# Performance work log

Measured on AMD Instinct MI355X. Metric: run time of the kernel, lower is better.

Reference implementation:

```python
import jax, jax.numpy as jnp
import numpy as np

B, U, D, H = 8, 256, 512, 32

def _layernorm(x, g, b, eps=1e-5):
    m = jnp.mean(x, axis=-1, keepdims=True)
    v = jnp.var(x, axis=-1, keepdims=True)
    return (x - m) * jax.lax.rsqrt(v + eps) * g + b

def setup_inputs() -> dict:
    key = jax.random.key(0)
    ks = jax.random.split(key, 12)
    s = 0.02
    return {
        "z_dyn": jax.random.normal(ks[0], (B, U, D), jnp.float32),
        "z_sem": jax.random.normal(ks[1], (B, U, D), jnp.float32),
        "te_w": jax.random.normal(ks[2], (H, D), jnp.float32) * s,
        "w_ih": jax.random.normal(ks[3], (3 * D, D), jnp.float32) * s,
        "w_hh": jax.random.normal(ks[4], (3 * D, D), jnp.float32) * s,
        "b_ih": jnp.zeros((3 * D,), jnp.float32),
        "b_hh": jnp.zeros((3 * D,), jnp.float32),
        "ln_g": jnp.ones((D,), jnp.float32),
        "ln_b": jnp.zeros((D,), jnp.float32),
        "ln2_g": jnp.ones((2 * D,), jnp.float32),
        "ln2_b": jnp.zeros((2 * D,), jnp.float32),
        "w1": jax.random.normal(ks[5], (D, 2 * D), jnp.float32) * s,
        "b1": jnp.zeros((D,), jnp.float32),
        "w2": jax.random.normal(ks[6], (D, D), jnp.float32) * s,
        "b2": jnp.zeros((D,), jnp.float32),
        "horizon": H,
    }

def reference(z_dyn, z_sem, te_w, w_ih, w_hh, b_ih, b_hh, ln_g, ln_b,
              ln2_g, ln2_b, w1, b1, w2, b2, horizon):
    b, u, d = z_dyn.shape
    h0 = z_dyn.reshape(b * u, d)
    sem = z_sem.reshape(b * u, d)
    idx = jnp.minimum(jnp.arange(horizon), te_w.shape[0] - 1)
    ts = te_w[idx]  # [horizon, d]

    def step(h, t):
        x = sem + t
        gi = x @ w_ih.T + b_ih   # [bu, 3d]
        gh = h @ w_hh.T + b_hh
        ir, iz, inn = jnp.split(gi, 3, axis=-1)
        hr, hz, hn = jnp.split(gh, 3, axis=-1)
        r = jax.nn.sigmoid(ir + hr)
        z = jax.nn.sigmoid(iz + hz)
        n = jnp.tanh(inn + r * hn)
        h_new = (1.0 - z) * n + z * h
        h_norm = _layernorm(h_new, ln_g, ln_b)
        cat = jnp.concatenate([sem, h_norm], axis=-1)
        hid = jax.nn.gelu(_layernorm(cat, ln2_g, ln2_b) @ w1.T + b1,
                          approximate=False)
        sem_h = sem + hid @ w2.T + b2
        return h_new, (h_norm, sem_h)

    _, (dyn, sems) = jax.lax.scan(step, h0, ts)  # [horizon, bu, d]
    dyn = dyn.reshape(horizon, b, u, d).transpose(1, 2, 0, 3)
    sems = sems.reshape(horizon, b, u, d).transpose(1, 2, 0, 3)
    return dyn, sems
```

## Files before the change

kernel.cpp:

```cpp
#include <hip/hip_runtime.h>
#include <math.h>


typedef unsigned short u16;
using bf16x8 = __attribute__((ext_vector_type(8))) short;
using f32x4  = __attribute__((ext_vector_type(4))) float;

#define DEV __device__ __forceinline__

constexpr int D   = 512;
constexpr int D3  = 1536;
constexpr int H   = 32;
constexpr int BU  = 2048;
constexpr long long OUT_HALF = (long long)BU * H * D;

DEV u16 f2bf(float x){
  union { float f; unsigned u; } c; c.f = x;
  unsigned u = c.u;
  u += 0x7fffu + ((u >> 16) & 1u);
  return (u16)(u >> 16);
}
DEV float bf2f(u16 b){
  union { unsigned u; float f; } c; c.u = ((unsigned)b) << 16; return c.f;
}

DEV void gload_lds16(const void* g, void* l){
  __builtin_amdgcn_global_load_lds(
      (const __attribute__((address_space(1))) void*)g,
      (__attribute__((address_space(3))) void*)l, 16, 0, 0);
}

DEV f32x4 mfma16(bf16x8 a, bf16x8 b, f32x4 c){
  return __builtin_amdgcn_mfma_f32_16x16x32_bf16(a, b, c, 0, 0, 0);
}

DEV float fsigm(float x){ return 1.f / (1.f + __expf(-x)); }
DEV float ftanh(float x){ return 1.f - 2.f / (1.f + __expf(2.f * x)); }

__global__ __launch_bounds__(256) void prep_kernel(
    const float* __restrict__ z_dyn, const float* __restrict__ z_sem,
    const float* __restrict__ te_w,  const float* __restrict__ w_ih,
    const float* __restrict__ w_hh,  const float* __restrict__ ln_g,
    const float* __restrict__ ln_b,  const float* __restrict__ ln2_g,
    const float* __restrict__ ln2_b, const float* __restrict__ w1,
    const float* __restrict__ b1,    const float* __restrict__ w2,
    float* __restrict__ h1, u16* __restrict__ hbh2, u16* __restrict__ hbl2,
    u16* __restrict__ sem_hi, u16* __restrict__ sem_lo,
    u16* __restrict__ wih_hi, u16* __restrict__ wih_lo,
    u16* __restrict__ whh_hi, u16* __restrict__ whh_lo,
    u16* __restrict__ W1s, u16* __restrict__ W1g, u16* __restrict__ w2bf,
    float* __restrict__ c1, float* __restrict__ c2p,
    float* __restrict__ d1, float* __restrict__ d2, float* __restrict__ Tg)
{
  int i = blockIdx.x * 256 + threadIdx.x;
  if (i < BU * D) {
    float hv = z_dyn[i];
    h1[i] = hv;
    u16 hh = f2bf(hv);
    hbh2[i] = hh;
    hbl2[i] = f2bf(hv - bf2f(hh));
    float sv = z_sem[i];
    u16 sh_ = f2bf(sv);
    sem_hi[i] = sh_;
    sem_lo[i] = f2bf(sv - bf2f(sh_));
  }
  if (i < D3 * D) {
    float wv = w_ih[i];
    u16 wh = f2bf(wv);
    wih_hi[i] = wh;
    wih_lo[i] = f2bf(wv - bf2f(wh));
    float uv = w_hh[i];
    u16 uh = f2bf(uv);
    whh_hi[i] = uh;
    whh_lo[i] = f2bf(uv - bf2f(uh));
  }
  if (i < D * D) {
    int k = i >> 9, j = i & 511;
    W1s[i]  = f2bf(w1[k * 1024 + j] * ln2_g[j]);
    w2bf[i] = f2bf(w2[i]);
  }
  if (i < D * 64) {
    int r = i >> 6, ln = i & 63;
    float sc1 = 0.f, sc2 = 0.f, sd1 = 0.f, sd2 = 0.f;
    #pragma unroll
    for (int jj = 0; jj < 8; ++jj) {
      int j = jj * 64 + ln;
      float wA = w1[r * 1024 + j];
      float wB = w1[r * 1024 + 512 + j];
      sc1 += wA * ln2_g[j] + wB * ln2_g[512 + j];
      sc2 += wA * ln2_b[j] + wB * ln2_b[512 + j];
      float wBg = wB * ln2_g[512 + j];
      float wg = wBg * ln_g[j];
      sd1 += wg;
      sd2 += wBg * ln_b[j];
      W1g[r * 512 + j] = f2bf(wg);
    }
    #pragma unroll
    for (int o = 1; o < 64; o <<= 1) {
      sc1 += __shfl_xor(sc1, o); sc2 += __shfl_xor(sc2, o);
      sd1 += __shfl_xor(sd1, o); sd2 += __shfl_xor(sd2, o);
    }
    if (ln == 0) {
      c1[r] = sc1;
      c2p[r] = sc2 + b1[r];
      d1[r] = sd1;
      d2[r] = sd2;
    }
  }
  if (i < H * D3) {
    int c = i >> 5, t = i & 31;
    float s = 0.f;
    for (int d0 = 0; d0 < D; ++d0) s += te_w[t * D + d0] * w_ih[c * D + d0];
    Tg[t * D3 + c] = s;
  }
}

__global__ __launch_bounds__(256) void rowstats_kernel(
    const float* __restrict__ sem, float* __restrict__ Ssem,
    float* __restrict__ Ssem2)
{
  const int wid = threadIdx.x >> 6, lane = threadIdx.x & 63;
  const int row = blockIdx.x * 4 + wid;
  const float* p = sem + (size_t)row * D + lane * 8;
  float4 a0 = *(const float4*)p;
  float4 a1 = *(const float4*)(p + 4);
  float s  = a0.x + a0.y + a0.z + a0.w + a1.x + a1.y + a1.z + a1.w;
  float s2 = a0.x*a0.x + a0.y*a0.y + a0.z*a0.z + a0.w*a0.w
           + a1.x*a1.x + a1.y*a1.y + a1.z*a1.z + a1.w*a1.w;
  #pragma unroll
  for (int o = 1; o < 64; o <<= 1) { s += __shfl_xor(s, o); s2 += __shfl_xor(s2, o); }
  if (lane == 0) { Ssem[row] = s; Ssem2[row] = s2; }
}

__global__ __launch_bounds__(256) void setup_kernel(
    const u16* __restrict__ sem_hi, const u16* __restrict__ sem_lo,
    const u16* __restrict__ wih_hi, const u16* __restrict__ wih_lo,
    const u16* __restrict__ W1s, float* __restrict__ G0,
    float* __restrict__ Psem, const float* __restrict__ b_ih)
{
  __shared__ __align__(16) char smem[32768];
  char* Ah = smem;
  char* Al = smem + 8192;
  char* Bh = smem + 16384;
  char* Bl = smem + 24576;
  const int tid = threadIdx.x, wid = tid >> 6, lane = tid & 63;
  const int wr = wid >> 1, wc = wid & 1;
  const bool isG0 = blockIdx.y < 24;
  const u16* Bsrc = isG0 ? wih_hi : W1s;
  const int row0 = blockIdx.x * 64;
  const int col0 = (isG0 ? blockIdx.y : blockIdx.y - 24) * 64;

  f32x4 acc[2][2] = {};
  for (int kt = 0; kt < 8; ++kt) {
    #pragma unroll
    for (int it = 0; it < 2; ++it) {
      int s = it * 256 + tid, pr = s >> 3, pc = s & 7;
      int lch = pc ^ (pr & 7);
      size_t aoff = (size_t)(row0 + pr) * D + kt * 64 + lch * 8;
      size_t boff = (size_t)(col0 + pr) * D + kt * 64 + lch * 8;
      gload_lds16(sem_hi + aoff, Ah + it * 4096 + wid * 1024);
      gload_lds16(Bsrc + boff,   Bh + it * 4096 + wid * 1024);
      if (isG0) {
        gload_lds16(sem_lo + aoff, Al + it * 4096 + wid * 1024);
        gload_lds16(wih_lo + boff, Bl + it * 4096 + wid * 1024);
      }
    }
    asm volatile("s_waitcnt vmcnt(0)" ::: "memory");
    __syncthreads();

    const int lc = lane & 15, hi2 = lane >> 4;
    #pragma unroll
    for (int kk = 0; kk < 2; ++kk) {
      int ch = kk * 4 + hi2;
      bf16x8 afh[2], afl[2], bfh[2], bfl[2];
      #pragma unroll
      for (int mi = 0; mi < 2; ++mi) {
        int r = wr * 32 + mi * 16 + lc;
        int o = r * 128 + ((ch ^ (r & 7)) << 4);
        afh[mi] = *(const bf16x8*)(Ah + o);
        if (isG0) afl[mi] = *(const bf16x8*)(Al + o);
      }
      #pragma unroll
      for (int ci = 0; ci < 2; ++ci) {
        int r = wc * 32 + ci * 16 + lc;
        int o = r * 128 + ((ch ^ (r & 7)) << 4);
        bfh[ci] = *(const bf16x8*)(Bh + o);
        if (isG0) bfl[ci] = *(const bf16x8*)(Bl + o);
      }
      #pragma unroll
      for (int mi = 0; mi < 2; ++mi)
        #pragma unroll
        for (int ci = 0; ci < 2; ++ci) {
          f32x4 a = acc[mi][ci];
          a = mfma16(afh[mi], bfh[ci], a);
          if (isG0) {
            a = mfma16(afl[mi], bfh[ci], a);
            a = mfma16(afh[mi], bfl[ci], a);
          }
          acc[mi][ci] = a;
        }
    }
    __syncthreads();
  }
  const int lj = lane >> 4, lc2 = lane & 15;
  #pragma unroll
  for (int mi = 0; mi < 2; ++mi)
    #pragma unroll
    for (int ci = 0; ci < 2; ++ci)
      #pragma unroll
      for (int j = 0; j < 4; ++j) {
        int row = row0 + wr * 32 + mi * 16 + lj * 4 + j;
        int col = col0 + wc * 32 + ci * 16 + lc2;
        float v = acc[mi][ci][j];
        if (isG0) G0[(size_t)row * D3 + col] = v + b_ih[col];
        else      Psem[(size_t)row * D + col] = v;
      }
}

__global__ __launch_bounds__(256, 4) void fused_kernel(
    int t,
    const u16* __restrict__ hbh_in, const u16* __restrict__ hbl_in,
    u16* __restrict__ hbh_out, u16* __restrict__ hbl_out,
    const float* __restrict__ hf_in, float* __restrict__ hf_out,
    const u16* __restrict__ whh_hi, const u16* __restrict__ whh_lo,
    const float* __restrict__ G0, const float* __restrict__ Tg,
    const float* __restrict__ bhh,
    float4* __restrict__ stats_w, float* __restrict__ dyn,
    const float* __restrict__ ln_g, const float* __restrict__ ln_b,
    const float* __restrict__ Ssem, const float* __restrict__ Ssem2,
    const u16* __restrict__ lbh,
    const float4* __restrict__ stats_r, const u16* __restrict__ W1g,
    const float* __restrict__ Psem, const float* __restrict__ d1,
    const float* __restrict__ d2, const float* __restrict__ c1,
    const float* __restrict__ c2p, u16* __restrict__ hid_w,
    const u16* __restrict__ hid_r, const u16* __restrict__ w2bf,
    const float* __restrict__ zsem, const float* __restrict__ b2,
    float* __restrict__ sems)
{
  __shared__ __align__(16) char smem[32768];
  const int bid = blockIdx.x;
  const int tid = threadIdx.x, wid = tid >> 6, lane = tid & 63;
  const int wr = wid >> 1, wc = wid & 1;
  const int lc = lane & 15, hi2 = lane >> 4;
  const int lj = lane >> 4, lc2 = lane & 15;

  if (bid < 512) {
    if (t >= H) return;
    const int row0 = (bid & 31) * 64;
    const int gc   = (bid >> 5) * 32;
    char* b0 = smem;
    char* b1 = smem + 16384;
    f32x4 acc[3][2] = {};

    const int gcol = gc + wc * 16 + lc2;

    float pre_gr[2][4], pre_gz[2][4], pre_gn[2][4], pre_hf[2][4];
    #pragma unroll
    for (int mi = 0; mi < 2; ++mi)
      #pragma unroll
      for (int j = 0; j < 4; ++j) {
        int row = row0 + wr * 32 + mi * 16 + lj * 4 + j;
        size_t g0i = (size_t)row * D3 + gcol;
        pre_gr[mi][j] = G0[g0i];
        pre_gz[mi][j] = G0[g0i + 512];
        pre_gn[mi][j] = G0[g0i + 1024];
        pre_hf[mi][j] = hf_in[(size_t)row * D + gcol];
      }

    auto stage = [&](char* base, int kt){
      { int row = tid >> 2;
        int ko = kt * 32 + (((tid & 3) ^ ((tid >> 3) & 3)) << 3);
        size_t off = (size_t)(row0 + row) * D + ko;
        gload_lds16(hbh_in + off, base + wid * 1024);
        gload_lds16(hbl_in + off, base + 4096 + wid * 1024);
      }
      #pragma unroll
      for (int it = 0; it < 2; ++it) {
        int s = it * 256 + tid;
        int row = s >> 2;
        int ko = kt * 32 + (((s & 3) ^ ((s >> 3) & 3)) << 3);
        const u16* src = (row < 96)
            ? whh_hi + (size_t)((row >> 5) * D + gc + (row & 31)) * D + ko
            : whh_lo + (size_t)(2 * D + gc + (row & 31)) * D + ko;
        gload_lds16(src, base + 8192 + it * 4096 + wid * 1024);
      }
    };

    auto compute = [&](const char* base){
      const int ch = hi2;
      bf16x8 afh[2], afl[2];
      #pragma unroll
      for (int mi = 0; mi < 2; ++mi) {
        int ra = wr * 32 + mi * 16 + lc;
        int ao = (ra >> 1) * 128 + (ra & 1) * 64
               + ((ch ^ ((ra >> 1) & 3)) << 4);
        afh[mi] = *(const bf16x8*)(base + ao);
        afl[mi] = *(const bf16x8*)(base + 4096 + ao);
      }
      const int rloc = wc * 16 + lc;
      #pragma unroll
      for (int g = 0; g < 3; ++g) {
        int rb = g * 32 + rloc;
        int bo = (rb >> 1) * 128 + (rb & 1) * 64
               + ((ch ^ ((rb >> 1) & 3)) << 4);
        bf16x8 bh = *(const bf16x8*)(base + 8192 + bo);
        #pragma unroll
        for (int mi = 0; mi < 2; ++mi) {
          f32x4 a = acc[g][mi];
          a = mfma16(afh[mi], bh, a);
          a = mfma16(afl[mi], bh, a);
          acc[g][mi] = a;
        }
      }
      { int rb = 96 + rloc;
        int bo = (rb >> 1) * 128 + (rb & 1) * 64
               + ((ch ^ ((rb >> 1) & 3)) << 4);
        bf16x8 bl = *(const bf16x8*)(base + 8192 + bo);
        #pragma unroll
        for (int mi = 0; mi < 2; ++mi)
          acc[2][mi] = mfma16(afh[mi], bl, acc[2][mi]);
      }
    };

    stage(b0, 0);
    stage(b1, 1);
    int buf = 0;
    for (int kt = 0; kt < 16; ++kt) {
      if (kt == 15) asm volatile("s_waitcnt vmcnt(0)" ::: "memory");
      else          asm volatile("s_waitcnt vmcnt(4)" ::: "memory");
      __builtin_amdgcn_s_barrier();
      compute(buf ? b1 : b0);
      __builtin_amdgcn_s_barrier();
      if (kt < 14) stage(buf ? b1 : b0, kt + 2);
      buf ^= 1;
    }

    const float br = bhh[gcol];
    const float bz = bhh[512 + gcol];
    const float bn = bhh[1024 + gcol];
    const float tr = Tg[t * D3 + gcol];
    const float tz = Tg[t * D3 + 512 + gcol];
    const float tn = Tg[t * D3 + 1024 + gcol];
    #pragma unroll
    for (int mi = 0; mi < 2; ++mi)
      #pragma unroll
      for (int j = 0; j < 4; ++j) {
        int row = row0 + wr * 32 + mi * 16 + lj * 4 + j;
        float gr = pre_gr[mi][j] + tr + acc[0][mi][j];
        float gz = pre_gz[mi][j] + tz + acc[1][mi][j];
        float gn = pre_gn[mi][j] + tn;
        float r = fsigm(gr + br);
        float z = fsigm(gz + bz);
        float n = ftanh(gn + r * (acc[2][mi][j] + bn));
        size_t hi_ = (size_t)row * D + gcol;
        float hnew = (1.f - z) * n + z * pre_hf[mi][j];
        hf_out[hi_] = hnew;
        u16 hh = f2bf(hnew);
        hbh_out[hi_] = hh;
        hbl_out[hi_] = f2bf(hnew - bf2f(hh));
      }
  } else if (bid < 768) {
    if (t < 2 || t > H + 1) return;
    const int i = bid - 512;
    const int row0 = (i & 31) * 64, col0 = (i >> 5) * 64;
    char* bufp[2] = { smem, smem + 16384 };
    f32x4 acc[2][2] = {};

    float pre_ps[2][2][4];
    float4 pre_st[2][4];
    #pragma unroll
    for (int mi = 0; mi < 2; ++mi)
      #pragma unroll
      for (int j = 0; j < 4; ++j) {
        int row = row0 + wr * 32 + mi * 16 + lj * 4 + j;
        pre_st[mi][j] = stats_r[row];
        #pragma unroll
        for (int ci = 0; ci < 2; ++ci) {
          int col = col0 + wc * 32 + ci * 16 + lc2;
          pre_ps[mi][ci][j] = Psem[(size_t)row * D + col];
        }
      }

    auto stage = [&](char* base, int kt){
      #pragma unroll
      for (int it = 0; it < 2; ++it) {
        int s = it * 256 + tid, pr = s >> 3, pc = s & 7;
        int lch = pc ^ (pr & 7);
        gload_lds16(lbh + (size_t)(row0 + pr) * D + kt * 64 + lch * 8,
                    base + it * 4096 + wid * 1024);
        gload_lds16(W1g + (size_t)(col0 + pr) * D + kt * 64 + lch * 8,
                    base + 8192 + it * 4096 + wid * 1024);
      }
    };

    stage(bufp[0], 0);
    __syncthreads();
    int buf = 0;
    for (int kt = 0; kt < 8; ++kt) {
      if (kt < 7) stage(bufp[buf ^ 1], kt + 1);
      const char* Ah = bufp[buf];
      const char* Bs = bufp[buf] + 8192;
      #pragma unroll
      for (int kk = 0; kk < 2; ++kk) {
        int ch = kk * 4 + hi2;
        bf16x8 afh[2], bf[2];
        #pragma unroll
        for (int mi = 0; mi < 2; ++mi) {
          int r = wr * 32 + mi * 16 + lc;
          afh[mi] = *(const bf16x8*)(Ah + r * 128 + ((ch ^ (r & 7)) << 4));
        }
        #pragma unroll
        for (int ci = 0; ci < 2; ++ci) {
          int r = wc * 32 + ci * 16 + lc;
          bf[ci] = *(const bf16x8*)(Bs + r * 128 + ((ch ^ (r & 7)) << 4));
        }
        #pragma unroll
        for (int mi = 0; mi < 2; ++mi)
          #pragma unroll
          for (int ci = 0; ci < 2; ++ci)
            acc[mi][ci] = mfma16(afh[mi], bf[ci], acc[mi][ci]);
      }
      __syncthreads();
      buf ^= 1;
    }

    #pragma unroll
    for (int mi = 0; mi < 2; ++mi)
      #pragma unroll
      for (int ci = 0; ci < 2; ++ci)
        #pragma unroll
        for (int j = 0; j < 4; ++j) {
          int row = row0 + wr * 32 + mi * 16 + lj * 4 + j;
          int col = col0 + wc * 32 + ci * 16 + lc2;
          float4 st = pre_st[mi][j];
          float hn_w1 = st.x * acc[mi][ci][j] - st.y * d1[col] + d2[col];
          float pre = st.z * (pre_ps[mi][ci][j] + hn_w1)
                      - st.w * c1[col] + c2p[col];
          float gl = 0.5f * pre * (1.f + erff(pre * 0.70710678118654752f));
          hid_w[(size_t)row * D + col] = f2bf(gl);
        }
  } else if (bid < 1024) {
    if (t < 3) return;
    const int ts = t - 3;
    const int i = bid - 768;
    const int row0 = (i & 31) * 64, col0 = (i >> 5) * 64;
    char* bufp[2] = { smem, smem + 16384 };
    f32x4 acc[2][2] = {};

    float pre_zs[2][2][4];
    #pragma unroll
    for (int mi = 0; mi < 2; ++mi)
      #pragma unroll
      for (int ci = 0; ci < 2; ++ci)
        #pragma unroll
        for (int j = 0; j < 4; ++j) {
          int row = row0 + wr * 32 + mi * 16 + lj * 4 + j;
          int col = col0 + wc * 32 + ci * 16 + lc2;
          pre_zs[mi][ci][j] = zsem[(size_t)row * D + col];
        }

    auto stage = [&](char* base, int kt){
      #pragma unroll
      for (int it = 0; it < 2; ++it) {
        int s = it * 256 + tid, pr = s >> 3, pc = s & 7;
        int lch = pc ^ (pr & 7);
        gload_lds16(hid_r + (size_t)(row0 + pr) * D + kt * 64 + lch * 8,
                    base + it * 4096 + wid * 1024);
        gload_lds16(w2bf + (size_t)(col0 + pr) * D + kt * 64 + lch * 8,
                    base + 8192 + it * 4096 + wid * 1024);
      }
    };

    stage(bufp[0], 0);
    __syncthreads();
    int buf = 0;
    for (int kt = 0; kt < 8; ++kt) {
      if (kt < 7) stage(bufp[buf ^ 1], kt + 1);
      const char* As = bufp[buf];
      const char* Bs = bufp[buf] + 8192;
      #pragma unroll
      for (int kk = 0; kk < 2; ++kk) {
        int ch = kk * 4 + hi2;
        bf16x8 af[2], bf[2];
        #pragma unroll
        for (int mi = 0; mi < 2; ++mi) {
          int r = wr * 32 + mi * 16 + lc;
          af[mi] = *(const bf16x8*)(As + r * 128 + ((ch ^ (r & 7)) << 4));
        }
        #pragma unroll
        for (int ci = 0; ci < 2; ++ci) {
          int r = wc * 32 + ci * 16 + lc;
          bf[ci] = *(const bf16x8*)(Bs + r * 128 + ((ch ^ (r & 7)) << 4));
        }
        #pragma unroll
        for (int mi = 0; mi < 2; ++mi)
          #pragma unroll
          for (int ci = 0; ci < 2; ++ci)
            acc[mi][ci] = mfma16(af[mi], bf[ci], acc[mi][ci]);
      }
      __syncthreads();
      buf ^= 1;
    }

    #pragma unroll
    for (int mi = 0; mi < 2; ++mi)
      #pragma unroll
      for (int ci = 0; ci < 2; ++ci)
        #pragma unroll
        for (int j = 0; j < 4; ++j) {
          int row = row0 + wr * 32 + mi * 16 + lj * 4 + j;
          int col = col0 + wc * 32 + ci * 16 + lc2;
          float v = pre_zs[mi][ci][j] + acc[mi][ci][j] + b2[col];
          __builtin_nontemporal_store(
              v, &sems[((size_t)row * H + ts) * D + col]);
        }
  } else {
    if (t < 1 || t > H) return;
    const int tt = t - 1;
    const int base = (bid - 1024) * 16 + wid * 4;
    const float4 g0 = *(const float4*)(ln_g + lane * 8);
    const float4 g1 = *(const float4*)(ln_g + lane * 8 + 4);
    const float4 b0 = *(const float4*)(ln_b + lane * 8);
    const float4 b1v = *(const float4*)(ln_b + lane * 8 + 4);
    const float gg[8] = {g0.x,g0.y,g0.z,g0.w,g1.x,g1.y,g1.z,g1.w};
    const float bb[8] = {b0.x,b0.y,b0.z,b0.w,b1v.x,b1v.y,b1v.z,b1v.w};

    for (int rr = 0; rr < 4; ++rr) {
      const int row = base + rr;
      const float* hp = hf_in + (size_t)row * D + lane * 8;
      float4 a0 = *(const float4*)hp, a1 = *(const float4*)(hp + 4);
      float h[8] = {a0.x, a0.y, a0.z, a0.w, a1.x, a1.y, a1.z, a1.w};
      float s1 = 0.f;
      #pragma unroll
      for (int k = 0; k < 8; ++k) s1 += h[k];
      #pragma unroll
      for (int o = 1; o < 64; o <<= 1) s1 += __shfl_xor(s1, o);
      float m1 = s1 * (1.f / 512.f);
      float s2 = 0.f;
      #pragma unroll
      for (int k = 0; k < 8; ++k) {
        float dv = h[k] - m1;
        s2 += dv * dv;
      }
      #pragma unroll
      for (int o = 1; o < 64; o <<= 1) s2 += __shfl_xor(s2, o);
      float rsd1 = rsqrtf(s2 * (1.f / 512.f) + 1e-5f);

      float hn[8];
      float sh = 0.f, sh2 = 0.f;
      #pragma unroll
      for (int k = 0; k < 8; ++k) {
        float x = (h[k] - m1) * rsd1 * gg[k] + bb[k];
        hn[k] = x; sh += x; sh2 += x * x;
      }
      float* dp = dyn + ((size_t)row * H + tt) * D + lane * 8;
      f32x4 v0 = {hn[0], hn[1], hn[2], hn[3]};
      f32x4 v1 = {hn[4], hn[5], hn[6], hn[7]};
      __builtin_nontemporal_store(v0, (f32x4*)dp);
      __builtin_nontemporal_store(v1, (f32x4*)(dp + 4));

      #pragma unroll
      for (int o = 1; o < 64; o <<= 1) {
        sh += __shfl_xor(sh, o); sh2 += __shfl_xor(sh2, o);
      }
      if (lane == 0) {
        float m2 = (Ssem[row] + sh) * (1.f / 1024.f);
        float vv = (Ssem2[row] + sh2) * (1.f / 1024.f) - m2 * m2;
        float rs2 = rsqrtf(vv + 1e-5f);
        stats_w[row] = make_float4(rsd1, m1 * rsd1, rs2, m2 * rs2);
      }
    }
  }
}

extern "C" void kernel_launch(void* const* d_in, const int* in_sizes, int n_in,
                              void* d_out, int out_size, void* d_ws, size_t ws_size,
                              hipStream_t stream)
{
  (void)in_sizes; (void)n_in; (void)out_size; (void)ws_size;
  const float* z_dyn = (const float*)d_in[0];
  const float* z_sem = (const float*)d_in[1];
  const float* te_w  = (const float*)d_in[2];
  const float* w_ih  = (const float*)d_in[3];
  const float* w_hh  = (const float*)d_in[4];
  const float* b_ih  = (const float*)d_in[5];
  const float* b_hh  = (const float*)d_in[6];
  const float* ln_g  = (const float*)d_in[7];
  const float* ln_b  = (const float*)d_in[8];
  const float* ln2_g = (const float*)d_in[9];
  const float* ln2_b = (const float*)d_in[10];
  const float* w1    = (const float*)d_in[11];
  const float* b1    = (const float*)d_in[12];
  const float* w2    = (const float*)d_in[13];
  const float* b2    = (const float*)d_in[14];

  char* ws = (char*)d_ws;
  const size_t MB = 1ull << 20;
  u16* hbh[3] = { (u16*)(ws + 0),      (u16*)(ws + 2 * MB),  (u16*)(ws + 4 * MB) };
  u16* hbl[3] = { (u16*)(ws + 6 * MB), (u16*)(ws + 8 * MB),  (u16*)(ws + 10 * MB) };
  float* G0     = (float*)(ws + 12 * MB);
  float* Psem   = (float*)(ws + 25 * MB);
  u16*  sem_hi  = (u16*)(ws + 29 * MB);
  u16*  sem_lo  = (u16*)(ws + 31 * MB);
  u16*  hid0    = (u16*)(ws + 33 * MB);
  u16*  hid1    = (u16*)(ws + 35 * MB);
  u16*  wih_hi  = (u16*)(ws + 37 * MB);
  u16*  wih_lo  = (u16*)(ws + 37 * MB + 1572864);
  u16*  whh_hi  = (u16*)(ws + 40 * MB);
  u16*  whh_lo  = (u16*)(ws + 40 * MB + 1572864);
  u16*  W1s     = (u16*)(ws + 43 * MB);
  u16*  W1g     = (u16*)(ws + 43 * MB + 524288);
  u16*  w2bf    = (u16*)(ws + 44 * MB);
  float* c1     = (float*)(ws + 45 * MB);
  float* c2p    = (float*)(ws + 45 * MB + 16384);
  float* d1     = (float*)(ws + 45 * MB + 32768);
  float* d2     = (float*)(ws + 45 * MB + 49152);
  float* Ssem   = (float*)(ws + 45 * MB + 65536);
  float* Ssem2  = (float*)(ws + 45 * MB + 81920);
  float4* stats0 = (float4*)(ws + 46 * MB);
  float4* stats1 = (float4*)(ws + 46 * MB + 32768);
  float* Tg     = (float*)(ws + 47 * MB);
  float* hf0    = (float*)(ws + 48 * MB);
  float* hf1    = (float*)(ws + 52 * MB);

  float* outp = (float*)d_out;
  float* out_dyn  = outp;
  float* out_sems = outp + OUT_HALF;

  prep_kernel<<<4096, 256, 0, stream>>>(
      z_dyn, z_sem, te_w, w_ih, w_hh, ln_g, ln_b, ln2_g, ln2_b, w1, b1, w2,
      hf1, hbh[2], hbl[2], sem_hi, sem_lo, wih_hi, wih_lo, whh_hi, whh_lo,
      W1s, W1g, w2bf, c1, c2p, d1, d2, Tg);
  rowstats_kernel<<<512, 256, 0, stream>>>(z_sem, Ssem, Ssem2);
  setup_kernel<<<dim3(32, 32), 256, 0, stream>>>(
      sem_hi, sem_lo, wih_hi, wih_lo, W1s, G0, Psem, b_ih);

  for (int t = 0; t <= H + 2; ++t) {
    int s_out  = ((t % 3) + 3) % 3;
    int s_in   = (((t - 1) % 3) + 3) % 3;
    int s_ln   = (((t - 2) % 3) + 3) % 3;
    float* hf_out      = (t & 1) ? hf1 : hf0;
    const float* hf_in = (t & 1) ? hf0 : hf1;
    float4* st_w = ((t - 1) & 1) ? stats1 : stats0;
    const float4* st_r = ((t - 2) & 1) ? stats1 : stats0;
    u16* hidw = ((t - 2) & 1) ? hid1 : hid0;
    const u16* hidr = ((t - 3) & 1) ? hid1 : hid0;

    fused_kernel<<<dim3(1152), dim3(256), 0, stream>>>(
        t,
        hbh[s_in], hbl[s_in], hbh[s_out], hbl[s_out],
        hf_in, hf_out,
        whh_hi, whh_lo, G0, Tg, b_hh,
        st_w, out_dyn, ln_g, ln_b, Ssem, Ssem2,
        hbh[s_ln], st_r, W1g, Psem, d1, d2, c1, c2p, hidw,
        hidr, w2bf, z_sem, b2, out_sems);
  }
}
```

Baseline: 769.6 us.

## Drop low-part MFMAs for r/z gates and simplify recurrent GEMM pipeline

The recurrent h@W_hh GEMM now applies the hi/lo split-bf16 correction of h only to the n gate. The r and z gates use the bf16 high part alone, which cuts the MFMA count per k-tile. The double-buffered pipeline moves from prefetch-distance-2 with manual vmcnt waits to a simpler prefetch-1 scheme with __syncthreads. The previous-h value is now read in the epilogue instead of being held in registers, which lowers register pressure at the cost of less load latency hiding and reduced precision in the r/z gates.

Measured after the change: 779.9 us. No clear change (+1.3%).

```diff
diff --git a/kernel.cpp b/kernel.cpp
--- a/kernel.cpp
+++ b/kernel.cpp
@@ -248,13 +248,11 @@
     if (t >= H) return;
     const int row0 = (bid & 31) * 64;
     const int gc   = (bid >> 5) * 32;
-    char* b0 = smem;
-    char* b1 = smem + 16384;
     f32x4 acc[3][2] = {};
 
     const int gcol = gc + wc * 16 + lc2;
 
-    float pre_gr[2][4], pre_gz[2][4], pre_gn[2][4], pre_hf[2][4];
+    float pre_gr[2][4], pre_gz[2][4], pre_gn[2][4];
     #pragma unroll
     for (int mi = 0; mi < 2; ++mi)
       #pragma unroll
@@ -264,10 +262,10 @@
         pre_gr[mi][j] = G0[g0i];
         pre_gz[mi][j] = G0[g0i + 512];
         pre_gn[mi][j] = G0[g0i + 1024];
-        pre_hf[mi][j] = hf_in[(size_t)row * D + gcol];
-      }
-
-    auto stage = [&](char* base, int kt){
+      }
+
+    auto stage = [&](int b, int kt){
+      char* base = smem + (b << 14);
       { int row = tid >> 2;
         int ko = kt * 32 + (((tid & 3) ^ ((tid >> 3) & 3)) << 3);
         size_t off = (size_t)(row0 + row) * D + ko;
@@ -286,7 +284,8 @@
       }
     };
 
-    auto compute = [&](const char* base){
+    auto compute = [&](int b){
+      const char* base = smem + (b << 14);
       const int ch = hi2;
       bf16x8 afh[2], afl[2];
       #pragma unroll
@@ -305,12 +304,12 @@
                + ((ch ^ ((rb >> 1) & 3)) << 4);
         bf16x8 bh = *(const bf16x8*)(base + 8192 + bo);
         #pragma unroll
-        for (int mi = 0; mi < 2; ++mi) {
-          f32x4 a = acc[g][mi];
-          a = mfma16(afh[mi], bh, a);
-          a = mfma16(afl[mi], bh, a);
-          acc[g][mi] = a;
-        }
+        for (int mi = 0; mi < 2; ++mi)
+          acc[g][mi] = mfma16(afh[mi], bh, acc[g][mi]);
+        if (g == 2)
+          #pragma unroll
+          for (int mi = 0; mi < 2; ++mi)
+            acc[2][mi] = mfma16(afl[mi], bh, acc[2][mi]);
       }
       { int rb = 96 + rloc;
         int bo = (rb >> 1) * 128 + (rb & 1) * 64
@@ -322,16 +321,13 @@
       }
     };
 
-    stage(b0, 0);
-    stage(b1, 1);
+    stage(0, 0);
+    __syncthreads();
     int buf = 0;
     for (int kt = 0; kt < 16; ++kt) {
-      if (kt == 15) asm volatile("s_waitcnt vmcnt(0)" ::: "memory");
-      else          asm volatile("s_waitcnt vmcnt(4)" ::: "memory");
-      __builtin_amdgcn_s_barrier();
-      compute(buf ? b1 : b0);
-      __builtin_amdgcn_s_barrier();
-      if (kt < 14) stage(buf ? b1 : b0, kt + 2);
+      if (kt < 15) stage(buf ^ 1, kt + 1);
+      compute(buf);
+      __syncthreads();
       buf ^= 1;
     }
 
@@ -353,7 +349,7 @@
         float z = fsigm(gz + bz);
         float n = ftanh(gn + r * (acc[2][mi][j] + bn));
         size_t hi_ = (size_t)row * D + gcol;
-        float hnew = (1.f - z) * n + z * pre_hf[mi][j];
+        float hnew = (1.f - z) * n + z * hf_in[hi_];
         hf_out[hi_] = hnew;
         u16 hh = f2bf(hnew);
         hbh_out[hi_] = hh;
@@ -363,7 +359,6 @@
     if (t < 2 || t > H + 1) return;
     const int i = bid - 512;
     const int row0 = (i & 31) * 64, col0 = (i >> 5) * 64;
-    char* bufp[2] = { smem, smem + 16384 };
     f32x4 acc[2][2] = {};
 
     float pre_ps[2][2][4];
@@ -381,7 +376,8 @@
         }
       }
 
-    auto stage = [&](char* base, int kt){
+    auto stage = [&](int b, int kt){
+      char* base = smem + (b << 14);
       #pragma unroll
       for (int it = 0; it < 2; ++it) {
         int s = it * 256 + tid, pr = s >> 3, pc = s & 7;
@@ -393,13 +389,13 @@
       }
     };
 
-    stage(bufp[0], 0);
+    stage(0, 0);
     __syncthreads();
     int buf = 0;
     for (int kt = 0; kt < 8; ++kt) {
-      if (kt < 7) stage(bufp[buf ^ 1], kt + 1);
-      const char* Ah = bufp[buf];
-      const char* Bs = bufp[buf] + 8192;
+      if (kt < 7) stage(buf ^ 1, kt + 1);
+      const char* Ah = smem + (buf << 14);
+      const char* Bs = Ah + 8192;
       #pragma unroll
       for (int kk = 0; kk < 2; ++kk) {
         int ch = kk * 4 + hi2;
@@ -444,7 +440,6 @@
     const int ts = t - 3;
     const int i = bid - 768;
     const int row0 = (i & 31) * 64, col0 = (i >> 5) * 64;
-    char* bufp[2] = { smem, smem + 16384 };
     f32x4 acc[2][2] = {};
 
     float pre_zs[2][2][4];
@@ -459,7 +454,8 @@
           pre_zs[mi][ci][j] = zsem[(size_t)row * D + col];
         }
 
-    auto stage = [&](char* base, int kt){
+    auto stage = [&](int b, int kt){
+      char* base = smem + (b << 14);
       #pragma unroll
       for (int it = 0; it < 2; ++it) {
         int s = it * 256 + tid, pr = s >> 3, pc = s & 7;
@@ -471,13 +467,13 @@
       }
     };
 
-    stage(bufp[0], 0);
+    stage(0, 0);
     __syncthreads();
     int buf = 0;
     for (int kt = 0; kt < 8; ++kt) {
-      if (kt < 7) stage(bufp[buf ^ 1], kt + 1);
-      const char* As = bufp[buf];
-      const char* Bs = bufp[buf] + 8192;
+      if (kt < 7) stage(buf ^ 1, kt + 1);
+      const char* As = smem + (buf << 14);
+      const char* Bs = As + 8192;
       #pragma unroll
       for (int kk = 0; kk < 2; ++kk) {
         int ch = kk * 4 + hi2;
```
